# Kernel tuning notes

Hardware: AMD Instinct MI355X
Metric: run time of the kernel (lower is better)

The kernel has to match this reference:

```python
import jax, jax.numpy as jnp
import numpy as np

ALPHA = 4.0  # spikingjelly surrogate.Sigmoid default

@jax.custom_vjp
def spike(x):
    return (x >= 0.0).astype(x.dtype)

def _spike_fwd(x):
    return spike(x), x

def _spike_bwd(x, g):
    s = jax.nn.sigmoid(ALPHA * x)
    return (g * ALPHA * s * (1.0 - s),)

spike.defvjp(_spike_fwd, _spike_bwd)

def lif(x, v0, v_th=1.0, tau=2.0):
    # Multi-step LIF over leading time axis. v' = v + (x - v)/tau; hard reset to 0; detach_reset.
    def step(v, xt):
        v = v + (xt - v) / tau
        s = spike(v - v_th)
        v = v * (1.0 - jax.lax.stop_gradient(s))
        return v, s
    v_end, s = jax.lax.scan(step, v0, x)
    return s, v_end

def bn_eval(x, gamma, beta, mean, var, eps=1e-5):
    # x: [T,B,C,N], stats over channel dim C (axis 2)
    inv = gamma / jnp.sqrt(var + eps)
    return x * inv.reshape(1, 1, -1, 1) + (beta - mean * inv).reshape(1, 1, -1, 1)

def setup_inputs() -> dict:
    key = jax.random.key(0)
    ks = jax.random.split(key, 24)
    T, B, C, H, W = 4, 16, 512, 16, 16
    d = {}
    d['x'] = jax.random.normal(ks[0], (T, B, C, H, W), dtype=jnp.float32)
    d['res_attn'] = jnp.zeros((1,), dtype=jnp.float32)
    sc = 1.0 / np.sqrt(C)
    for i, p in enumerate(['q', 'k', 'v']):
        d[p + '_w'] = jax.random.normal(ks[1 + i], (C, C), dtype=jnp.float32) * sc
    names = ['q', 'k', 'v', 'p']
    for i, p in enumerate(names):
        d[p + '_gamma'] = jax.random.uniform(ks[4 + i], (C,), minval=0.8, maxval=1.2, dtype=jnp.float32)
        d[p + '_beta'] = jax.random.normal(ks[8 + i], (C,), dtype=jnp.float32) * 0.1
        d[p + '_mean'] = jax.random.normal(ks[12 + i], (C,), dtype=jnp.float32) * 0.1
        d[p + '_var'] = jax.random.uniform(ks[16 + i], (C,), minval=0.5, maxval=1.5, dtype=jnp.float32)
    d['p_w'] = jax.random.normal(ks[20], (C, C), dtype=jnp.float32) * sc
    d['p_b'] = jax.random.normal(ks[21], (C,), dtype=jnp.float32) * 0.02
    return d

def reference(x, res_attn, q_w, q_gamma, q_beta, q_mean, q_var,
              k_w, k_gamma, k_beta, k_mean, k_var,
              v_w, v_gamma, v_beta, v_mean, v_var,
              p_w, p_b, p_gamma, p_beta, p_mean, p_var):
    T, B, C, H, W = x.shape
    N = H * W
    xf = x.reshape(T, B, C, N)
    v0 = jnp.zeros((B, C, N), dtype=x.dtype)

    def qkv_branch(w, g, b, m, va):
        y = jnp.einsum('oc,tbcn->tbon', w, xf)  # 1x1 conv over flattened T*B
        y = bn_eval(y, g, b, m, va)
        s, _ = lif(y, v0)
        return s

    q = qkv_branch(q_w, q_gamma, q_beta, q_mean, q_var)
    k = qkv_branch(k_w, k_gamma, k_beta, k_mean, k_var)
    v = qkv_branch(v_w, v_gamma, v_beta, v_mean, v_var)

    kv = jnp.einsum('tbcn,tbcm->tbnm', k, v)           # k^T @ v : [T,B,N,N]
    a = jnp.einsum('tbcn,tbnm->tbcm', q, kv) * 0.125   # q @ (k^T v), scale
    a, _ = lif(a, v0, v_th=0.5)                        # attn_lif

    y = jnp.einsum('oc,tbcn->tbon', p_w, a) + p_b.reshape(1, 1, -1, 1)
    y = bn_eval(y, p_gamma, p_beta, p_mean, p_var).reshape(T, B, C, H, W)

    v0_sp = jnp.zeros((B, C, H, W), dtype=x.dtype)
    s1, v_end = lif(y, v0_sp)      # first proj_lif call
    s2, _ = lif(s1, v_end)         # second proj_lif call: membrane state persists (stateful node)
    return s2, v
```

## Files before the change

kernel.cpp:

```cpp
#include <hip/hip_runtime.h>
#include <hip/hip_bf16.h>

#define TT 4
#define BB 16
#define CC 512
#define NN 256

typedef short short8 __attribute__((ext_vector_type(8)));
typedef _Float16 h8 __attribute__((ext_vector_type(8)));
typedef float f32x4 __attribute__((ext_vector_type(4)));
typedef float fl4 __attribute__((ext_vector_type(4)));
typedef unsigned short us4 __attribute__((ext_vector_type(4)));

__device__ __forceinline__ unsigned short bf_hi(float x) {
    unsigned u = __float_as_uint(x);
    return (unsigned short)((u + 0x7FFFu + ((u >> 16) & 1u)) >> 16);
}
__device__ __forceinline__ float bf_f(unsigned short h) {
    return __uint_as_float(((unsigned)h) << 16);
}
__device__ __forceinline__ void glds16(const void* g, void* l) {
    __builtin_amdgcn_global_load_lds(
        (const __attribute__((address_space(1))) unsigned int*)g,
        (__attribute__((address_space(3))) unsigned int*)l, 16, 0, 0);
}
__device__ __forceinline__ int csw(int c, int rkey) {
    return (c & ~63) | ((((c >> 3) & 7) ^ (rkey & 7)) << 3) | (c & 7);
}

__global__ __launch_bounds__(256) void prep_k(
    const float* __restrict__ x,
    const float* __restrict__ w0, const float* __restrict__ w1,
    const float* __restrict__ w2, const float* __restrict__ w3,
    unsigned short* __restrict__ xh, unsigned short* __restrict__ xl,
    unsigned short* __restrict__ wsplit)
{
    const int bid = blockIdx.x;
    const int tid = threadIdx.x;
    if (bid < 4096) {
        __shared__ float Tt[64][33];
        const int tb = bid >> 6, rem = bid & 63;
        const int c0 = (rem >> 3) * 64, n0 = (rem & 7) * 32;
        const int t = tb >> 4, b = tb & 15;
        {
            int row = tid >> 2, seg = tid & 3;
            const float* sp = x + ((size_t)tb * CC + c0 + row) * NN + n0 + seg * 8;
            fl4 v0 = *(const fl4*)sp;
            fl4 v1 = *(const fl4*)(sp + 4);
#pragma unroll
            for (int j = 0; j < 4; ++j) {
                Tt[row][seg * 8 + j] = v0[j];
                Tt[row][seg * 8 + 4 + j] = v1[j];
            }
        }
        __syncthreads();
        {
            int n = tid >> 3, co = tid & 7;
            int c = c0 + co * 8;
            short8 hi, lo;
#pragma unroll
            for (int j = 0; j < 8; ++j) {
                float f = Tt[co * 8 + j][n];
                unsigned short h = bf_hi(f);
                hi[j] = (short)h;
                lo[j] = (short)bf_hi(f - bf_f(h));
            }
            int nn = n0 + n;
            int key = (nn & 1) * 4 + t;
            size_t dst = (((size_t)b * NN + nn) * TT + t) * CC
                       + (c & ~63) + (((((c >> 3) & 7) ^ (key & 7))) << 3);
            *(short8*)(xh + dst) = hi;
            *(short8*)(xl + dst) = lo;
        }
    } else {
        const int wb = bid - 4096;
        const int m = wb >> 7;
        const int idx = wb & 127;
        const float* src = (m == 0) ? w0 : (m == 1) ? w1 : (m == 2) ? w2 : w3;
        unsigned short* dh = wsplit + (size_t)m * 2 * CC * CC;
        unsigned short* dl = dh + (size_t)CC * CC;
        const int flat = idx * 2048 + tid * 8;
        const int o = flat >> 9, c = flat & 511;
        const float* sp = src + flat;
        fl4 v0 = *(const fl4*)sp;
        fl4 v1 = *(const fl4*)(sp + 4);
        short8 hi, lo;
#pragma unroll
        for (int j = 0; j < 8; ++j) {
            float f = (j < 4) ? v0[j] : v1[j - 4];
            unsigned short h = bf_hi(f);
            hi[j] = (short)h;
            lo[j] = (short)bf_hi(f - bf_f(h));
        }
        size_t dst = (size_t)o * CC + (c & ~63) + ((((c >> 3) & 7) ^ (o & 7)) << 3);
        *(short8*)(dh + dst) = hi;
        *(short8*)(dl + dst) = lo;
    }
}

__global__ __launch_bounds__(256) void gemm_qkv_f(
    const unsigned short* __restrict__ w8,
    const unsigned short* __restrict__ Bh, const unsigned short* __restrict__ Bl,
    const float* __restrict__ qg, const float* __restrict__ qb,
    const float* __restrict__ qm, const float* __restrict__ qva,
    const float* __restrict__ kg, const float* __restrict__ kbe,
    const float* __restrict__ km, const float* __restrict__ kva,
    const float* __restrict__ vg, const float* __restrict__ vb,
    const float* __restrict__ vm, const float* __restrict__ vva,
    const float* __restrict__ qw, const float* __restrict__ kw,
    const float* __restrict__ vw, const float* __restrict__ xf,
    unsigned short* __restrict__ qo, unsigned short* __restrict__ ktr,
    unsigned short* __restrict__ vtr, float* __restrict__ outv)
{
    const int bid = blockIdx.x;
    const int orig = (bid & 7) * 384 + (bid >> 3);
    const int cb = orig / 12;
    const int ob = orig - cb * 12;
    const int mat = ob >> 2;
    const int o0 = (ob & 3) * 128;
    const int col0 = cb * 64;
    const int b  = cb >> 4;
    const int n0 = (cb & 15) * 16;
    const unsigned short* Ah = w8 + (size_t)mat * 2 * CC * CC;
    const unsigned short* Al = Ah + (size_t)CC * CC;

    const int tid = threadIdx.x, lane = tid & 63, wid = tid >> 6;
    const int l16 = lane & 15, kb = lane >> 4;
    const int sx = l16 & 7;

    __shared__ __align__(16) char raw[49152];

    const unsigned short* gsrc =
        (wid == 0) ? Ah + (size_t)o0 * CC :
        (wid == 1) ? Al + (size_t)o0 * CC :
        (wid == 2) ? Bh + (size_t)col0 * CC :
                     Bl + (size_t)col0 * CC;
    char* ldsb = raw + ((wid < 2) ? wid * 16384 : 32768 + (wid - 2) * 8192);
    const int nglds = (wid < 2) ? 16 : 8;
    const int srow = lane >> 3, sslot = lane & 7;

    f32x4 acc[2][4];
#pragma unroll
    for (int r = 0; r < 2; ++r)
#pragma unroll
        for (int c = 0; c < 4; ++c) acc[r][c] = (f32x4){0.f, 0.f, 0.f, 0.f};

    for (int ks = 0; ks < 8; ++ks) {
        const int k0 = ks * 64;
#pragma unroll
        for (int i = 0; i < 16; ++i)
            if (i < nglds)
                glds16(gsrc + (size_t)(i * 8 + srow) * CC + k0 + sslot * 8,
                       ldsb + i * 1024);
        __syncthreads();
#pragma unroll
        for (int ksub = 0; ksub < 2; ++ksub) {
            const int soff = ((ksub * 4 + kb) ^ sx) << 4;
            short8 ah[2], al[2], bh[4], bl[4];
#pragma unroll
            for (int r = 0; r < 2; ++r) {
                const int ra = (wid * 32 + r * 16 + l16) * 128 + soff;
                ah[r] = *(const short8*)(raw + ra);
                al[r] = *(const short8*)(raw + 16384 + ra);
            }
#pragma unroll
            for (int c = 0; c < 4; ++c) {
                const int rb = (c * 16 + l16) * 128 + soff;
                bh[c] = *(const short8*)(raw + 32768 + rb);
                bl[c] = *(const short8*)(raw + 40960 + rb);
            }
#pragma unroll
            for (int r = 0; r < 2; ++r)
#pragma unroll
                for (int c = 0; c < 4; ++c)
                    acc[r][c] = __builtin_amdgcn_mfma_f32_16x16x32_bf16(ah[r], bh[c], acc[r][c], 0, 0, 0);
#pragma unroll
            for (int r = 0; r < 2; ++r)
#pragma unroll
                for (int c = 0; c < 4; ++c)
                    acc[r][c] = __builtin_amdgcn_mfma_f32_16x16x32_bf16(al[r], bh[c], acc[r][c], 0, 0, 0);
#pragma unroll
            for (int r = 0; r < 2; ++r)
#pragma unroll
                for (int c = 0; c < 4; ++c)
                    acc[r][c] = __builtin_amdgcn_mfma_f32_16x16x32_bf16(ah[r], bl[c], acc[r][c], 0, 0, 0);
        }
        __syncthreads();
    }

    float* Yf = (float*)raw;
#pragma unroll
    for (int r = 0; r < 2; ++r)
#pragma unroll
        for (int c = 0; c < 4; ++c) {
            const int col = c * 16 + l16;
#pragma unroll
            for (int g = 0; g < 4; ++g) {
                const int row = wid * 32 + r * 16 + kb * 4 + g;
                Yf[row * 64 + (col ^ (((row >> 2) & 7) << 2))] = acc[r][c][g];
            }
        }
    __syncthreads();

    const float* gg = (mat == 0) ? qg : (mat == 1) ? kg : vg;
    const float* be = (mat == 0) ? qb : (mat == 1) ? kbe : vb;
    const float* mu = (mat == 0) ? qm : (mat == 1) ? km : vm;
    const float* va = (mat == 0) ? qva : (mat == 1) ? kva : vva;
    const float* wsel = (mat == 0) ? qw : (mat == 1) ? kw : vw;

    const int lo2  = tid >> 3;
    const int rsel = (tid >> 2) & 1;
    const int ln2  = tid & 3;
    const float M1 = 2e-4f;

    float inv[2], bbv[2];
#pragma unroll
    for (int i = 0; i < 2; ++i) {
        int oo = o0 + lo2 * 4 + rsel * 2 + i;
        double invd = (double)gg[oo] / sqrt((double)va[oo] + 1e-5);
        inv[i] = (float)invd;
        bbv[i] = (float)((double)be[oo] - (double)mu[oo] * invd);
    }

    unsigned long long s1b = 0;
    unsigned fmask = 0;
#pragma unroll
    for (int i = 0; i < 2; ++i) {
        const int row = lo2 * 4 + rsel * 2 + i;
        const int rk = ((row >> 2) & 7) << 2;
#pragma unroll
        for (int j = 0; j < 4; ++j) {
            fl4 yv = *(const fl4*)&Yf[row * 64 + (((ln2 * 4 + j) * 4) ^ rk)];
            float vv = 0.f;
#pragma unroll
            for (int t = 0; t < TT; ++t) {
                float yy = yv[t] * inv[i] + bbv[i];
                vv += (yy - vv) * 0.5f;
                float d = vv - 1.0f;
                if (d < M1 && d > -M1) fmask |= 1u << (i * 4 + j);
                if (d >= 0.0f) { s1b |= 1ull << ((i * 4 + j) * 4 + t); vv = 0.f; }
            }
        }
    }

    unsigned long long ball = __ballot(fmask != 0);
    while (ball) {
        int src = __ffsll(ball) - 1;
        ball &= ball - 1;
        unsigned fm = (unsigned)__shfl((int)fmask, src);
        int slo2 = wid * 8 + (src >> 3);
        int srsel = (src >> 2) & 1, sln = src & 3;
        while (fm) {
            int cell = __ffs(fm) - 1;
            fm &= fm - 1;
            int ci = cell >> 2, cj = cell & 3;
            int oo = o0 + slo2 * 4 + srsel * 2 + ci, nn = n0 + sln * 4 + cj;
            double a0 = 0, a1 = 0, a2 = 0, a3 = 0;
            const float* wrow = wsel + (size_t)oo * CC;
            for (int c = lane; c < CC; c += 64) {
                double wv = (double)wrow[c];
                a0 += wv * (double)xf[(((size_t)(0 * BB + b) * CC + c) * NN) + nn];
                a1 += wv * (double)xf[(((size_t)(1 * BB + b) * CC + c) * NN) + nn];
                a2 += wv * (double)xf[(((size_t)(2 * BB + b) * CC + c) * NN) + nn];
                a3 += wv * (double)xf[(((size_t)(3 * BB + b) * CC + c) * NN) + nn];
            }
#pragma unroll
            for (int off = 32; off > 0; off >>= 1) {
                a0 += __shfl_xor(a0, off);
                a1 += __shfl_xor(a1, off);
                a2 += __shfl_xor(a2, off);
                a3 += __shfl_xor(a3, off);
            }
            if (lane == src) {
                double inv_ = (double)gg[oo] / sqrt((double)va[oo] + 1e-5);
                double bb_  = (double)be[oo] - (double)mu[oo] * inv_;
                s1b &= ~(0xFull << (cell * 4));
                double aa[4] = {a0, a1, a2, a3};
                double vv = 0.0;
#pragma unroll
                for (int t = 0; t < TT; ++t) {
                    double yy = aa[t] * inv_ + bb_;
                    vv += (yy - vv) * 0.5;
                    if (vv >= 1.0) { s1b |= 1ull << (cell * 4 + t); vv = 0.0; }
                }
            }
        }
    }

    if (mat == 0) {
#pragma unroll
        for (int t = 0; t < TT; ++t) {
            const size_t tb = (size_t)(t * BB + b);
#pragma unroll
            for (int i = 0; i < 2; ++i) {
                us4 pk;
#pragma unroll
                for (int j = 0; j < 4; ++j)
                    pk[j] = ((s1b >> ((i * 4 + j) * 4 + t)) & 1ull) ? (unsigned short)0x3C00 : (unsigned short)0;
                *(us4*)(qo + (tb * CC + o0 + lo2 * 4 + rsel * 2 + i) * NN + n0 + ln2 * 4) = pk;
            }
        }
    } else {
        unsigned short* tr = (mat == 1) ? ktr : vtr;
        unsigned short* Tss = (unsigned short*)raw;
        __syncthreads();
#pragma unroll
        for (int t = 0; t < TT; ++t)
#pragma unroll
            for (int j = 0; j < 4; ++j) {
                unsigned p0 = ((s1b >> ((0 * 4 + j) * 4 + t)) & 1ull) ? 0x3F80u : 0u;
                unsigned p1 = ((s1b >> ((1 * 4 + j) * 4 + t)) & 1ull) ? 0x3F80u : 0u;
                *(unsigned*)&Tss[t * 2176 + (ln2 * 4 + j) * 136 + lo2 * 4 + rsel * 2] =
                    p0 | (p1 << 16);
            }
        __syncthreads();
        {
            const int nrow = tid >> 4, seg = tid & 15;
#pragma unroll
            for (int t = 0; t < TT; ++t) {
                const unsigned short* sp = Tss + t * 2176 + nrow * 136 + seg * 8;
                short8 w0 = *(const short8*)sp;
                unsigned short* dst = tr + ((size_t)(t * BB + b) * NN + n0 + nrow) * CC + o0 + seg * 8;
                *(short8*)dst = w0;
            }
        }
        if (mat == 2) {
#pragma unroll
            for (int t = 0; t < TT; ++t) {
                const size_t tb = (size_t)(t * BB + b);
#pragma unroll
                for (int i = 0; i < 2; ++i) {
                    fl4 f;
#pragma unroll
                    for (int j = 0; j < 4; ++j)
                        f[j] = ((s1b >> ((i * 4 + j) * 4 + t)) & 1ull) ? 1.f : 0.f;
                    *(fl4*)(outv + (tb * CC + o0 + lo2 * 4 + rsel * 2 + i) * NN + n0 + ln2 * 4) = f;
                }
            }
        }
    }
}

__global__ __launch_bounds__(256) void gemm_p_f(
    const unsigned short* __restrict__ Ah, const unsigned short* __restrict__ Al,
    const unsigned short* __restrict__ Bhb,
    const float* __restrict__ gg, const float* __restrict__ be,
    const float* __restrict__ mu, const float* __restrict__ va,
    const float* __restrict__ pb, const float* __restrict__ pw,
    const unsigned short* __restrict__ abf, float* __restrict__ out)
{
    const int bid = blockIdx.x;
    const int orig = (bid & 7) * 128 + (bid >> 3);
    const int ob = orig & 3, cb = orig >> 2;
    const int o0 = ob * 128, col0 = cb * 64;
    const int b = cb >> 4, n0 = (cb & 15) * 16;
    const int tid = threadIdx.x, lane = tid & 63, wid = tid >> 6;
    const int l16 = lane & 15, kb = lane >> 4;
    const int sx = l16 & 7;

    __shared__ __align__(16) char raw[40960];

    const unsigned short* gsrc;
    char* ldsb;
    int nglds;
    if (wid == 0)      { gsrc = Ah + (size_t)o0 * CC;  ldsb = raw;          nglds = 16; }
    else if (wid == 1) { gsrc = Al + (size_t)o0 * CC;  ldsb = raw + 16384;  nglds = 16; }
    else {
        gsrc = Bhb + (size_t)(col0 + (wid - 2) * 32) * CC;
        ldsb = raw + 32768 + (wid - 2) * 4096;
        nglds = 4;
    }
    const int srow = lane >> 3, sslot = lane & 7;

    f32x4 acc[2][4];
#pragma unroll
    for (int r = 0; r < 2; ++r)
#pragma unroll
        for (int c = 0; c < 4; ++c) acc[r][c] = (f32x4){0.f, 0.f, 0.f, 0.f};

    for (int ks = 0; ks < 8; ++ks) {
        const int k0 = ks * 64;
#pragma unroll
        for (int i = 0; i < 16; ++i)
            if (i < nglds)
                glds16(gsrc + (size_t)(i * 8 + srow) * CC + k0 + sslot * 8,
                       ldsb + i * 1024);
        __syncthreads();
#pragma unroll
        for (int ksub = 0; ksub < 2; ++ksub) {
            const int soff = ((ksub * 4 + kb) ^ sx) << 4;
            short8 ah[2], al[2], bh[4];
#pragma unroll
            for (int r = 0; r < 2; ++r) {
                const int ra = (wid * 32 + r * 16 + l16) * 128 + soff;
                ah[r] = *(const short8*)(raw + ra);
                al[r] = *(const short8*)(raw + 16384 + ra);
            }
#pragma unroll
            for (int c = 0; c < 4; ++c) {
                const int rb = (c * 16 + l16) * 128 + soff;
                bh[c] = *(const short8*)(raw + 32768 + rb);
            }
#pragma unroll
            for (int r = 0; r < 2; ++r)
#pragma unroll
                for (int c = 0; c < 4; ++c)
                    acc[r][c] = __builtin_amdgcn_mfma_f32_16x16x32_bf16(ah[r], bh[c], acc[r][c], 0, 0, 0);
#pragma unroll
            for (int r = 0; r < 2; ++r)
#pragma unroll
                for (int c = 0; c < 4; ++c)
                    acc[r][c] = __builtin_amdgcn_mfma_f32_16x16x32_bf16(al[r], bh[c], acc[r][c], 0, 0, 0);
        }
        __syncthreads();
    }

    float* Yf = (float*)raw;
#pragma unroll
    for (int r = 0; r < 2; ++r)
#pragma unroll
        for (int c = 0; c < 4; ++c) {
            const int col = c * 16 + l16;
#pragma unroll
            for (int g = 0; g < 4; ++g) {
                const int row = wid * 32 + r * 16 + kb * 4 + g;
                Yf[row * 64 + (col ^ (((row >> 2) & 7) << 2))] = acc[r][c][g];
            }
        }
    __syncthreads();

    const int lo2  = tid >> 3;
    const int rsel = (tid >> 2) & 1;
    const int ln2  = tid & 3;
    const float M1 = 2e-4f;

    float inv[2], bbv[2], pbo[2];
#pragma unroll
    for (int i = 0; i < 2; ++i) {
        int oo = o0 + lo2 * 4 + rsel * 2 + i;
        double invd = (double)gg[oo] / sqrt((double)va[oo] + 1e-5);
        inv[i] = (float)invd;
        bbv[i] = (float)((double)be[oo] - (double)mu[oo] * invd);
        pbo[i] = pb[oo];
    }

    unsigned long long s2b = 0;
    unsigned fmask = 0;
#pragma unroll
    for (int i = 0; i < 2; ++i) {
        const int row = lo2 * 4 + rsel * 2 + i;
        const int rk = ((row >> 2) & 7) << 2;
#pragma unroll
        for (int j = 0; j < 4; ++j) {
            fl4 yv = *(const fl4*)&Yf[row * 64 + (((ln2 * 4 + j) * 4) ^ rk)];
            float vv = 0.f;
            unsigned s1loc = 0;
#pragma unroll
            for (int t = 0; t < TT; ++t) {
                float yy = (yv[t] + pbo[i]) * inv[i] + bbv[i];
                vv += (yy - vv) * 0.5f;
                float d = vv - 1.0f;
                if (d < M1 && d > -M1) fmask |= 1u << (i * 4 + j);
                if (d >= 0.0f) { s1loc |= 1u << t; vv = 0.f; }
            }
            float v2 = vv;
#pragma unroll
            for (int t = 0; t < TT; ++t) {
                float s1 = ((s1loc >> t) & 1u) ? 1.f : 0.f;
                v2 += (s1 - v2) * 0.5f;
                float d = v2 - 1.0f;
                if (d < M1 && d > -M1) fmask |= 1u << (i * 4 + j);
                if (d >= 0.0f) { s2b |= 1ull << ((i * 4 + j) * 4 + t); v2 = 0.f; }
            }
        }
    }

    unsigned long long ball = __ballot(fmask != 0);
    while (ball) {
        int src = __ffsll(ball) - 1;
        ball &= ball - 1;
        unsigned fm = (unsigned)__shfl((int)fmask, src);
        int slo2 = wid * 8 + (src >> 3);
        int srsel = (src >> 2) & 1, sln = src & 3;
        while (fm) {
            int cell = __ffs(fm) - 1;
            fm &= fm - 1;
            int ci = cell >> 2, cj = cell & 3;
            int oo = o0 + slo2 * 4 + srsel * 2 + ci, nn = n0 + sln * 4 + cj;
            double a0 = 0, a1 = 0, a2 = 0, a3 = 0;
            const float* wrow = pw + (size_t)oo * CC;
            const int key0 = (nn & 1) * 4;
            for (int c = lane; c < CC; c += 64) {
                double wv = (double)wrow[c];
                size_t rb = ((size_t)b * NN + nn) * TT;
                if (abf[(rb + 0) * CC + csw(c, key0 + 0)]) a0 += wv;
                if (abf[(rb + 1) * CC + csw(c, key0 + 1)]) a1 += wv;
                if (abf[(rb + 2) * CC + csw(c, key0 + 2)]) a2 += wv;
                if (abf[(rb + 3) * CC + csw(c, key0 + 3)]) a3 += wv;
            }
#pragma unroll
            for (int off = 32; off > 0; off >>= 1) {
                a0 += __shfl_xor(a0, off);
                a1 += __shfl_xor(a1, off);
                a2 += __shfl_xor(a2, off);
                a3 += __shfl_xor(a3, off);
            }
            if (lane == src) {
                double inv_ = (double)gg[oo] / sqrt((double)va[oo] + 1e-5);
                double bb_  = (double)be[oo] - (double)mu[oo] * inv_;
                double pb_  = (double)pb[oo];
                s2b &= ~(0xFull << (cell * 4));
                double aa[4] = {a0, a1, a2, a3};
                double vv = 0.0;
                unsigned s1loc = 0;
#pragma unroll
                for (int t = 0; t < TT; ++t) {
                    double yy = (aa[t] + pb_) * inv_ + bb_;
                    vv += (yy - vv) * 0.5;
                    if (vv >= 1.0) { s1loc |= 1u << t; vv = 0.0; }
                }
                double v2 = vv;
#pragma unroll
                for (int t = 0; t < TT; ++t) {
                    double s1 = ((s1loc >> t) & 1u) ? 1.0 : 0.0;
                    v2 += (s1 - v2) * 0.5;
                    if (v2 >= 1.0) { s2b |= 1ull << (cell * 4 + t); v2 = 0.0; }
                }
            }
        }
    }

#pragma unroll
    for (int t = 0; t < TT; ++t) {
        const size_t tb = (size_t)(t * BB + b);
#pragma unroll
        for (int i = 0; i < 2; ++i) {
            fl4 f;
#pragma unroll
            for (int j = 0; j < 4; ++j)
                f[j] = ((s2b >> ((i * 4 + j) * 4 + t)) & 1ull) ? 1.f : 0.f;
            *(fl4*)(out + (tb * CC + o0 + lo2 * 4 + rsel * 2 + i) * NN + n0 + ln2 * 4) = f;
        }
    }
}

__global__ __launch_bounds__(256) void k2_kv(
    const unsigned short* __restrict__ kt, const unsigned short* __restrict__ vt,
    unsigned short* __restrict__ kvf)
{
    const int m0 = blockIdx.x * 64, n0 = blockIdx.y * 64, tb = blockIdx.z;
    const int tid = threadIdx.x, lane = tid & 63, wid = tid >> 6;
    const int wn = wid >> 1, wm = wid & 1;
    const int l16 = lane & 15, kb = lane >> 4;
    __shared__ unsigned short Kt[64][72];
    __shared__ unsigned short Vt[64][72];
    f32x4 acc[2][2];
#pragma unroll
    for (int a = 0; a < 2; ++a)
#pragma unroll
        for (int c = 0; c < 2; ++c) acc[a][c] = (f32x4){0.f, 0.f, 0.f, 0.f};

    for (int ks = 0; ks < 8; ++ks) {
        const int c0 = ks * 64;
#pragma unroll
        for (int i = tid; i < 1024; i += 256) {
            int which = i >> 9, r = (i >> 3) & 63, s = i & 7;
            const unsigned short* sp = (which ? vt : kt) +
                ((size_t)tb * NN + (which ? m0 : n0) + r) * CC + c0 + s * 8;
            unsigned short (*dst)[72] = which ? Vt : Kt;
            *(short8*)(&dst[r][s * 8]) = *(const short8*)sp;
        }
        __syncthreads();
#pragma unroll
        for (int ksub = 0; ksub < 2; ++ksub) {
            const int co = ksub * 32 + kb * 8;
            short8 a0 = *(const short8*)&Kt[wn * 32 + l16][co];
            short8 a1 = *(const short8*)&Kt[wn * 32 + 16 + l16][co];
            short8 b0 = *(const short8*)&Vt[wm * 32 + l16][co];
            short8 b1 = *(const short8*)&Vt[wm * 32 + 16 + l16][co];
            acc[0][0] = __builtin_amdgcn_mfma_f32_16x16x32_bf16(a0, b0, acc[0][0], 0, 0, 0);
            acc[0][1] = __builtin_amdgcn_mfma_f32_16x16x32_bf16(a0, b1, acc[0][1], 0, 0, 0);
            acc[1][0] = __builtin_amdgcn_mfma_f32_16x16x32_bf16(a1, b0, acc[1][0], 0, 0, 0);
            acc[1][1] = __builtin_amdgcn_mfma_f32_16x16x32_bf16(a1, b1, acc[1][1], 0, 0, 0);
        }
        __syncthreads();
    }
#pragma unroll
    for (int fr = 0; fr < 2; ++fr)
#pragma unroll
        for (int fc = 0; fc < 2; ++fc) {
            int n = n0 + wn * 32 + fr * 16 + kb * 4;
            int m = m0 + wm * 32 + fc * 16 + l16;
            us4 pk;
#pragma unroll
            for (int rg = 0; rg < 4; ++rg) {
                union { _Float16 h; unsigned short u; } cv;
                cv.h = (_Float16)acc[fr][fc][rg];
                pk[rg] = cv.u;
            }
            *(us4*)&kvf[((size_t)tb * NN + m) * NN + n] = pk;
        }
}

__global__ __launch_bounds__(256) void k3_attn(
    const unsigned short* __restrict__ qf, const unsigned short* __restrict__ kvf,
    unsigned short* __restrict__ abf)
{
    const int c0 = blockIdx.x * 64, m0 = blockIdx.y * 64, b = blockIdx.z;
    const int tid = threadIdx.x, lane = tid & 63, wid = tid >> 6;
    const int wc = wid >> 1, wm = wid & 1;
    const int l16 = lane & 15, kb = lane >> 4;
    __shared__ unsigned short Qt[TT][64][40];
    __shared__ unsigned short Mt[TT][64][40];
    f32x4 acc[TT][2][2];
#pragma unroll
    for (int t = 0; t < TT; ++t)
#pragma unroll
        for (int fr = 0; fr < 2; ++fr)
#pragma unroll
            for (int fc = 0; fc < 2; ++fc) acc[t][fr][fc] = (f32x4){0.f, 0.f, 0.f, 0.f};

    for (int ks = 0; ks < 8; ++ks) {
        const int nk0 = ks * 32;
#pragma unroll
        for (int i = tid; i < 2048; i += 256) {
            int which = i >> 10, rem = i & 1023;
            int t = rem >> 8, r = (rem >> 2) & 63, s = rem & 3;
            if (which == 0) {
                const unsigned short* sp = qf + ((size_t)(t * BB + b) * CC + c0 + r) * NN + nk0 + s * 8;
                *(short8*)(&Qt[t][r][s * 8]) = *(const short8*)sp;
            } else {
                const unsigned short* sp = kvf + ((size_t)(t * BB + b) * NN + m0 + r) * NN + nk0 + s * 8;
                *(short8*)(&Mt[t][r][s * 8]) = *(const short8*)sp;
            }
        }
        __syncthreads();
#pragma unroll
        for (int t = 0; t < TT; ++t) {
            h8 a0 = *(const h8*)&Qt[t][wc * 32 + l16][kb * 8];
            h8 a1 = *(const h8*)&Qt[t][wc * 32 + 16 + l16][kb * 8];
            h8 b0 = *(const h8*)&Mt[t][wm * 32 + l16][kb * 8];
            h8 b1 = *(const h8*)&Mt[t][wm * 32 + 16 + l16][kb * 8];
            acc[t][0][0] = __builtin_amdgcn_mfma_f32_16x16x32_f16(a0, b0, acc[t][0][0], 0, 0, 0);
            acc[t][0][1] = __builtin_amdgcn_mfma_f32_16x16x32_f16(a0, b1, acc[t][0][1], 0, 0, 0);
            acc[t][1][0] = __builtin_amdgcn_mfma_f32_16x16x32_f16(a1, b0, acc[t][1][0], 0, 0, 0);
            acc[t][1][1] = __builtin_amdgcn_mfma_f32_16x16x32_f16(a1, b1, acc[t][1][1], 0, 0, 0);
        }
        __syncthreads();
    }

#pragma unroll
    for (int fr = 0; fr < 2; ++fr)
#pragma unroll
        for (int fc = 0; fc < 2; ++fc) {
            const int m = m0 + wm * 32 + fc * 16 + l16;
            const int cbase = c0 + wc * 32 + fr * 16 + kb * 4;
            const int key0 = (m & 1) * 4;
            us4 pk[TT];
#pragma unroll
            for (int rg = 0; rg < 4; ++rg) {
                float vv = 0.f;
#pragma unroll
                for (int t = 0; t < TT; ++t) {
                    float a = acc[t][fr][fc][rg] * 0.125f;
                    vv += (a - vv) * 0.5f;
                    if (vv >= 0.5f) { pk[t][rg] = 0x3F80; vv = 0.f; }
                    else pk[t][rg] = 0;
                }
            }
#pragma unroll
            for (int t = 0; t < TT; ++t)
                *(us4*)&abf[(((size_t)b * NN + m) * TT + t) * CC + csw(cbase, key0 + t)] = pk[t];
        }
}

extern "C" void kernel_launch(void* const* d_in, const int* in_sizes, int n_in,
                              void* d_out, int out_size, void* d_ws, size_t ws_size,
                              hipStream_t stream)
{
    const float* x    = (const float*)d_in[0];
    const float* q_w  = (const float*)d_in[2];
    const float* k_w  = (const float*)d_in[3];
    const float* v_w  = (const float*)d_in[4];
    const float* q_g  = (const float*)d_in[5];
    const float* q_b  = (const float*)d_in[6];
    const float* q_m  = (const float*)d_in[7];
    const float* q_v  = (const float*)d_in[8];
    const float* k_g  = (const float*)d_in[9];
    const float* k_b  = (const float*)d_in[10];
    const float* k_m  = (const float*)d_in[11];
    const float* k_v  = (const float*)d_in[12];
    const float* v_g  = (const float*)d_in[13];
    const float* v_b  = (const float*)d_in[14];
    const float* v_m  = (const float*)d_in[15];
    const float* v_v  = (const float*)d_in[16];
    const float* p_g  = (const float*)d_in[17];
    const float* p_be = (const float*)d_in[18];
    const float* p_m  = (const float*)d_in[19];
    const float* p_v  = (const float*)d_in[20];
    const float* p_w  = (const float*)d_in[21];
    const float* p_b  = (const float*)d_in[22];

    const size_t ELEMS = (size_t)TT * BB * CC * NN;
    float* out_s2 = (float*)d_out;
    float* out_v  = out_s2 + ELEMS;

    unsigned char* ws8 = (unsigned char*)d_ws;
    unsigned short* xh   = (unsigned short*)ws8;
    unsigned short* xl   = (unsigned short*)(ws8 + 16777216ull);
    unsigned short* w8   = (unsigned short*)(ws8 + 33554432ull);
    unsigned short* qf16 = (unsigned short*)(ws8 + 37748736ull);
    unsigned short* kt   = (unsigned short*)(ws8 + 54525952ull);
    unsigned short* vt   = (unsigned short*)(ws8 + 71303168ull);
    unsigned short* kvf  = (unsigned short*)(ws8 + 88080384ull);
    unsigned short* abf  = (unsigned short*)(ws8 + 104857600ull);

    const size_t WSZ = (size_t)CC * CC;
    unsigned short* wph = w8 + 6 * WSZ;
    unsigned short* wpl = w8 + 7 * WSZ;

    dim3 blk(256);
    prep_k<<<4608, blk, 0, stream>>>(x, q_w, k_w, v_w, p_w, xh, xl, w8);

    gemm_qkv_f<<<3072, blk, 0, stream>>>(w8, xh, xl,
                                         q_g, q_b, q_m, q_v,
                                         k_g, k_b, k_m, k_v,
                                         v_g, v_b, v_m, v_v,
                                         q_w, k_w, v_w, x,
                                         qf16, kt, vt, out_v);

    k2_kv<<<dim3(4, 4, 64), blk, 0, stream>>>(kt, vt, kvf);
    k3_attn<<<dim3(8, 4, 16), blk, 0, stream>>>(qf16, kvf, abf);

    gemm_p_f<<<1024, blk, 0, stream>>>(wph, wpl, abf,
                                       p_g, p_be, p_m, p_v, p_b, p_w,
                                       abf, out_s2);
}
```

Before: 188.9 us.

## Double-buffer QKV GEMM LDS loads with larger 128x128 tiles and 512 threads

Changes the QKV GEMM block tile from 128x64 to 128x128 using 8 waves (512 threads), halving the grid. The K loop now double-buffers global-to-LDS loads in 128KB of shared memory, so the next k-slice is prefetched while MFMAs run on the current one. Epilogue indexing is updated for the wider tile. The large LDS footprint limits residency to one block per CU, and the epilogue mapping changes may expose indexing bugs.

```diff
diff --git a/kernel.cpp b/kernel.cpp
--- a/kernel.cpp
+++ b/kernel.cpp
@@ -98,7 +98,7 @@
     }
 }
 
-__global__ __launch_bounds__(256) void gemm_qkv_f(
+__global__ __launch_bounds__(512) void gemm_qkv_f(
     const unsigned short* __restrict__ w8,
     const unsigned short* __restrict__ Bh, const unsigned short* __restrict__ Bl,
     const float* __restrict__ qg, const float* __restrict__ qb,
@@ -113,76 +113,89 @@
     unsigned short* __restrict__ vtr, float* __restrict__ outv)
 {
     const int bid = blockIdx.x;
-    const int orig = (bid & 7) * 384 + (bid >> 3);
+    const int orig = (bid & 7) * 192 + (bid >> 3);
     const int cb = orig / 12;
     const int ob = orig - cb * 12;
     const int mat = ob >> 2;
     const int o0 = (ob & 3) * 128;
-    const int col0 = cb * 64;
-    const int b  = cb >> 4;
-    const int n0 = (cb & 15) * 16;
+    const int col0 = cb * 128;
+    const int b  = cb >> 3;
+    const int n0 = (cb & 7) * 32;
     const unsigned short* Ah = w8 + (size_t)mat * 2 * CC * CC;
     const unsigned short* Al = Ah + (size_t)CC * CC;
 
     const int tid = threadIdx.x, lane = tid & 63, wid = tid >> 6;
     const int l16 = lane & 15, kb = lane >> 4;
     const int sx = l16 & 7;
-
-    __shared__ __align__(16) char raw[49152];
-
-    const unsigned short* gsrc =
-        (wid == 0) ? Ah + (size_t)o0 * CC :
-        (wid == 1) ? Al + (size_t)o0 * CC :
-        (wid == 2) ? Bh + (size_t)col0 * CC :
-                     Bl + (size_t)col0 * CC;
-    char* ldsb = raw + ((wid < 2) ? wid * 16384 : 32768 + (wid - 2) * 8192);
-    const int nglds = (wid < 2) ? 16 : 8;
+    const int wr = wid >> 2;
+    const int wc = wid & 3;
+
+    __shared__ __align__(16) char raw[131072];
+
+    const int sect = wid >> 1;
+    const int half = wid & 1;
     const int srow = lane >> 3, sslot = lane & 7;
-
-    f32x4 acc[2][4];
-#pragma unroll
-    for (int r = 0; r < 2; ++r)
-#pragma unroll
-        for (int c = 0; c < 4; ++c) acc[r][c] = (f32x4){0.f, 0.f, 0.f, 0.f};
+    const unsigned short* sectbase =
+        (sect == 0) ? Ah + (size_t)(o0 + half * 64) * CC :
+        (sect == 1) ? Al + (size_t)(o0 + half * 64) * CC :
+        (sect == 2) ? Bh + (size_t)(col0 + half * 64) * CC :
+                      Bl + (size_t)(col0 + half * 64) * CC;
+    const unsigned short* gsrc = sectbase + (size_t)srow * CC + sslot * 8;
+    const int sectoff = sect * 16384 + half * 8192;
+
+    f32x4 acc[4][2];
+#pragma unroll
+    for (int r = 0; r < 4; ++r)
+#pragma unroll
+        for (int c = 0; c < 2; ++c) acc[r][c] = (f32x4){0.f, 0.f, 0.f, 0.f};
+
+    {
+        char* db = raw + sectoff;
+#pragma unroll
+        for (int i = 0; i < 8; ++i)
+            glds16(gsrc + (size_t)i * 8 * CC, db + i * 1024);
+    }
+    __syncthreads();
 
     for (int ks = 0; ks < 8; ++ks) {
-        const int k0 = ks * 64;
-#pragma unroll
-        for (int i = 0; i < 16; ++i)
-            if (i < nglds)
-                glds16(gsrc + (size_t)(i * 8 + srow) * CC + k0 + sslot * 8,
-                       ldsb + i * 1024);
-        __syncthreads();
+        char* buf = raw + (ks & 1) * 65536;
+        if (ks < 7) {
+            char* db = raw + ((ks + 1) & 1) * 65536 + sectoff;
+            const unsigned short* gs = gsrc + (ks + 1) * 64;
+#pragma unroll
+            for (int i = 0; i < 8; ++i)
+                glds16(gs + (size_t)i * 8 * CC, db + i * 1024);
+        }
 #pragma unroll
         for (int ksub = 0; ksub < 2; ++ksub) {
             const int soff = ((ksub * 4 + kb) ^ sx) << 4;
-            short8 ah[2], al[2], bh[4], bl[4];
-#pragma unroll
-            for (int r = 0; r < 2; ++r) {
-                const int ra = (wid * 32 + r * 16 + l16) * 128 + soff;
-                ah[r] = *(const short8*)(raw + ra);
-                al[r] = *(const short8*)(raw + 16384 + ra);
-            }
-#pragma unroll
-            for (int c = 0; c < 4; ++c) {
-                const int rb = (c * 16 + l16) * 128 + soff;
-                bh[c] = *(const short8*)(raw + 32768 + rb);
-                bl[c] = *(const short8*)(raw + 40960 + rb);
-            }
-#pragma unroll
-            for (int r = 0; r < 2; ++r)
-#pragma unroll
-                for (int c = 0; c < 4; ++c)
+            short8 ah[4], al[4], bh[2], bl[2];
+#pragma unroll
+            for (int r = 0; r < 4; ++r) {
+                const int ra = (wr * 64 + r * 16 + l16) * 128 + soff;
+                ah[r] = *(const short8*)(buf + ra);
+                al[r] = *(const short8*)(buf + 16384 + ra);
+            }
+#pragma unroll
+            for (int c = 0; c < 2; ++c) {
+                const int rb = (wc * 32 + c * 16 + l16) * 128 + soff;
+                bh[c] = *(const short8*)(buf + 32768 + rb);
+                bl[c] = *(const short8*)(buf + 49152 + rb);
+            }
+#pragma unroll
+            for (int r = 0; r < 4; ++r)
+#pragma unroll
+                for (int c = 0; c < 2; ++c)
                     acc[r][c] = __builtin_amdgcn_mfma_f32_16x16x32_bf16(ah[r], bh[c], acc[r][c], 0, 0, 0);
 #pragma unroll
-            for (int r = 0; r < 2; ++r)
-#pragma unroll
-                for (int c = 0; c < 4; ++c)
+            for (int r = 0; r < 4; ++r)
+#pragma unroll
+                for (int c = 0; c < 2; ++c)
                     acc[r][c] = __builtin_amdgcn_mfma_f32_16x16x32_bf16(al[r], bh[c], acc[r][c], 0, 0, 0);
 #pragma unroll
-            for (int r = 0; r < 2; ++r)
-#pragma unroll
-                for (int c = 0; c < 4; ++c)
+            for (int r = 0; r < 4; ++r)
+#pragma unroll
+                for (int c = 0; c < 2; ++c)
                     acc[r][c] = __builtin_amdgcn_mfma_f32_16x16x32_bf16(ah[r], bl[c], acc[r][c], 0, 0, 0);
         }
         __syncthreads();
@@ -190,14 +203,14 @@
 
     float* Yf = (float*)raw;
 #pragma unroll
-    for (int r = 0; r < 2; ++r)
-#pragma unroll
-        for (int c = 0; c < 4; ++c) {
-            const int col = c * 16 + l16;
+    for (int r = 0; r < 4; ++r)
+#pragma unroll
+        for (int c = 0; c < 2; ++c) {
+            const int col = wc * 32 + c * 16 + l16;
 #pragma unroll
             for (int g = 0; g < 4; ++g) {
-                const int row = wid * 32 + r * 16 + kb * 4 + g;
-                Yf[row * 64 + (col ^ (((row >> 2) & 7) << 2))] = acc[r][c][g];
+                const int row = wr * 64 + r * 16 + kb * 4 + g;
+                Yf[row * 128 + (col ^ (((row >> 2) & 7) << 2))] = acc[r][c][g];
             }
         }
     __syncthreads();
@@ -208,9 +221,9 @@
     const float* va = (mat == 0) ? qva : (mat == 1) ? kva : vva;
     const float* wsel = (mat == 0) ? qw : (mat == 1) ? kw : vw;
 
-    const int lo2  = tid >> 3;
-    const int rsel = (tid >> 2) & 1;
-    const int ln2  = tid & 3;
+    const int lo2  = tid >> 4;
+    const int rsel = (tid >> 3) & 1;
+    const int ln2  = tid & 7;
     const float M1 = 2e-4f;
 
     float inv[2], bbv[2];
@@ -230,7 +243,7 @@
         const int rk = ((row >> 2) & 7) << 2;
 #pragma unroll
         for (int j = 0; j < 4; ++j) {
-            fl4 yv = *(const fl4*)&Yf[row * 64 + (((ln2 * 4 + j) * 4) ^ rk)];
+            fl4 yv = *(const fl4*)&Yf[row * 128 + (((ln2 * 4 + j) * 4) ^ rk)];
             float vv = 0.f;
 #pragma unroll
             for (int t = 0; t < TT; ++t) {
@@ -248,8 +261,8 @@
         int src = __ffsll(ball) - 1;
         ball &= ball - 1;
         unsigned fm = (unsigned)__shfl((int)fmask, src);
-        int slo2 = wid * 8 + (src >> 3);
-        int srsel = (src >> 2) & 1, sln = src & 3;
+        int slo2 = wid * 4 + (src >> 4);
+        int srsel = (src >> 3) & 1, sln = src & 7;
         while (fm) {
             int cell = __ffs(fm) - 1;
             fm &= fm - 1;
@@ -310,7 +323,7 @@
             for (int j = 0; j < 4; ++j) {
                 unsigned p0 = ((s1b >> ((0 * 4 + j) * 4 + t)) & 1ull) ? 0x3F80u : 0u;
                 unsigned p1 = ((s1b >> ((1 * 4 + j) * 4 + t)) & 1ull) ? 0x3F80u : 0u;
-                *(unsigned*)&Tss[t * 2176 + (ln2 * 4 + j) * 136 + lo2 * 4 + rsel * 2] =
+                *(unsigned*)&Tss[t * 4352 + (ln2 * 4 + j) * 136 + lo2 * 4 + rsel * 2] =
                     p0 | (p1 << 16);
             }
         __syncthreads();
@@ -318,7 +331,7 @@
             const int nrow = tid >> 4, seg = tid & 15;
 #pragma unroll
             for (int t = 0; t < TT; ++t) {
-                const unsigned short* sp = Tss + t * 2176 + nrow * 136 + seg * 8;
+                const unsigned short* sp = Tss + t * 4352 + nrow * 136 + seg * 8;
                 short8 w0 = *(const short8*)sp;
                 unsigned short* dst = tr + ((size_t)(t * BB + b) * NN + n0 + nrow) * CC + o0 + seg * 8;
                 *(short8*)dst = w0;
@@ -720,14 +733,15 @@
     unsigned short* wpl = w8 + 7 * WSZ;
 
     dim3 blk(256);
+    dim3 blk512(512);
     prep_k<<<4608, blk, 0, stream>>>(x, q_w, k_w, v_w, p_w, xh, xl, w8);
 
-    gemm_qkv_f<<<3072, blk, 0, stream>>>(w8, xh, xl,
-                                         q_g, q_b, q_m, q_v,
-                                         k_g, k_b, k_m, k_v,
-                                         v_g, v_b, v_m, v_v,
-                                         q_w, k_w, v_w, x,
-                                         qf16, kt, vt, out_v);
+    gemm_qkv_f<<<1536, blk512, 0, stream>>>(w8, xh, xl,
+                                            q_g, q_b, q_m, q_v,
+                                            k_g, k_b, k_m, k_v,
+                                            v_g, v_b, v_m, v_v,
+                                            q_w, k_w, v_w, x,
+                                            qf16, kt, vt, out_v);
 
     k2_kv<<<dim3(4, 4, 64), blk, 0, stream>>>(kt, vt, kvf);
     k3_attn<<<dim3(8, 4, 16), blk, 0, stream>>>(qf16, kvf, abf);
```

Result: slower. 202.8 us (+7.4%).
